# Performance work log

Hardware: AMD Instinct MI355X
Metric: run time of the kernel (lower is better)

The kernel has to match this reference:

```python
import jax, jax.numpy as jnp
import numpy as np

H = 12          # num attention heads
D_HEAD = 64     # head size (768 / 12)
P = 2           # power-law exponent
C = 5.0         # score shift
EPS = 1e-10


def setup_inputs() -> dict:
    key = jax.random.key(0)
    ks = jax.random.split(key, 8)
    B, S, Dm = 32, 512, 768
    scale = 1.0 / np.sqrt(Dm)
    return {
        "hidden_states": jax.random.normal(ks[0], (B, S, Dm), dtype=jnp.float32),
        "attention_mask": jnp.ones((B, 1, 1, S), dtype=jnp.float32),
        "Wq": jax.random.normal(ks[1], (Dm, Dm), dtype=jnp.float32) * scale,
        "bq": jnp.zeros((Dm,), dtype=jnp.float32),
        "Wk": jax.random.normal(ks[2], (Dm, Dm), dtype=jnp.float32) * scale,
        "bk": jnp.zeros((Dm,), dtype=jnp.float32),
        "Wv": jax.random.normal(ks[3], (Dm, Dm), dtype=jnp.float32) * scale,
        "bv": jnp.zeros((Dm,), dtype=jnp.float32),
    }


def _heads(x, B, S):
    # [B, S, H*d] -> [B, H, S, d]
    return x.reshape(B, S, H, D_HEAD).transpose(0, 2, 1, 3)


def reference(hidden_states, attention_mask, Wq, bq, Wk, bk, Wv, bv):
    B, S, Dm = hidden_states.shape
    q = _heads(hidden_states @ Wq + bq, B, S)
    k = _heads(hidden_states @ Wk + bk, B, S)
    v = _heads(hidden_states @ Wv + bv, B, S)

    inv_sqrt_d = 1.0 / (np.sqrt(D_HEAD) + 1e-10)
    scores = jnp.einsum("bhqd,bhkd->bhqk", q, k) * inv_sqrt_d  # [B,H,S,S]

    # Power-law attention (Powerformer, distill=0 branch)
    probs = jnp.power(scores + C, P)
    probs = probs / (jnp.sum(probs, axis=-1, keepdims=True) + EPS)
    probs = probs * attention_mask  # mask multiplied after normalization

    ctx = jnp.einsum("bhqk,bhkd->bhqd", probs, v)  # [B,H,S,d]
    ctx = ctx.transpose(0, 2, 1, 3).reshape(B, S, Dm)
    return ctx
```

## Files before the change

### kernel.cpp

```cpp
#include <hip/hip_runtime.h>

typedef __attribute__((ext_vector_type(8))) _Float16 half8;
typedef __attribute__((ext_vector_type(4))) _Float16 half4;
typedef __attribute__((ext_vector_type(4))) float f32x4;

#define MFMA_K32(a, b, c) __builtin_amdgcn_mfma_f32_16x16x32_f16((a), (b), (c), 0, 0, 0)
#define MFMA_K16(a, b, c) __builtin_amdgcn_mfma_f32_16x16x16f16((a), (b), (c), 0, 0, 0)

__device__ inline void async16(const _Float16* g, _Float16* l) {
    __builtin_amdgcn_global_load_lds(
        (const __attribute__((address_space(1))) void*)g,
        (__attribute__((address_space(3))) void*)l, 16, 0, 0);
}


__global__ __launch_bounds__(256) void xcast(const float* __restrict__ X,
                                             _Float16* __restrict__ Xh)
{
    size_t idx = ((size_t)blockIdx.x * 256 + threadIdx.x) * 8;
    float4 a = *(const float4*)(X + idx);
    float4 c = *(const float4*)(X + idx + 4);
    half8 hv;
    hv[0] = (_Float16)a.x; hv[1] = (_Float16)a.y;
    hv[2] = (_Float16)a.z; hv[3] = (_Float16)a.w;
    hv[4] = (_Float16)c.x; hv[5] = (_Float16)c.y;
    hv[6] = (_Float16)c.z; hv[7] = (_Float16)c.w;
    *(half8*)(Xh + idx) = hv;
}

__global__ __launch_bounds__(256) void wcast_kernel(
    const float* __restrict__ W0, const float* __restrict__ W1,
    const float* __restrict__ W2,
    _Float16* __restrict__ T0, _Float16* __restrict__ T1,
    _Float16* __restrict__ T2)
{
    int z = blockIdx.z;
    const float* W = (z == 0) ? W0 : (z == 1) ? W1 : W2;
    _Float16* T = (z == 0) ? T0 : (z == 1) ? T1 : T2;
    __shared__ float tile[32][33];
    int n0 = blockIdx.x * 32, k0 = blockIdx.y * 32;
    int tx = threadIdx.x & 31, ty = threadIdx.x >> 5;
#pragma unroll
    for (int r = 0; r < 4; ++r)
        tile[ty + 8 * r][tx] = W[(size_t)(k0 + ty + 8 * r) * 768 + n0 + tx];
    __syncthreads();
#pragma unroll
    for (int r = 0; r < 4; ++r)
        T[(size_t)(n0 + ty + 8 * r) * 768 + k0 + tx] =
            (_Float16)tile[tx][ty + 8 * r];
}

__global__ __launch_bounds__(256) void qkv_gemm(
    const _Float16* __restrict__ Xh,
    const _Float16* __restrict__ W0, const _Float16* __restrict__ W1,
    const _Float16* __restrict__ W2,
    const float* __restrict__ b0, const float* __restrict__ b1,
    const float* __restrict__ b2,
    const float* __restrict__ mask,
    _Float16* __restrict__ Qo, _Float16* __restrict__ Ko,
    _Float16* __restrict__ Vo)
{
    int z = blockIdx.y / 6;
    int n0 = (blockIdx.y % 6) * 128;
    int m0 = blockIdx.x * 128;
    const _Float16* Wt = (z == 0) ? W0 : (z == 1) ? W1 : W2;
    const float* bias = (z == 0) ? b0 : (z == 1) ? b1 : b2;

    __shared__ __attribute__((aligned(16))) _Float16 As[128 * 64];
    __shared__ __attribute__((aligned(16))) _Float16 Bs[128 * 64];

    int t = threadIdx.x;
    int wave = t >> 6, lane = t & 63, quad = lane >> 4, l16 = lane & 15;
    int wm = (wave & 1) * 64, wn = (wave >> 1) * 64;

    int srow = t >> 3;
    int sg = (t & 7) ^ (srow & 7);

    const _Float16* gA = Xh + (size_t)(m0 + srow) * 768 + sg * 8;
    const _Float16* gB = Wt + (size_t)(n0 + srow) * 768 + sg * 8;
    _Float16* lA = As + t * 8;
    _Float16* lB = Bs + t * 8;

    f32x4 acc[4][4] = {};

    for (int k0 = 0; k0 < 768; k0 += 64) {
#pragma unroll
        for (int q = 0; q < 4; ++q) {
            async16(gA + (size_t)q * 32 * 768 + k0, lA + q * 2048);
            async16(gB + (size_t)q * 32 * 768 + k0, lB + q * 2048);
        }
        __syncthreads();
#pragma unroll
        for (int ks = 0; ks < 2; ++ks) {
            half8 af[4], bf[4];
#pragma unroll
            for (int i = 0; i < 4; ++i) {
                int row = wm + i * 16 + l16;
                af[i] = *(const half8*)&As[row * 64 +
                                           (((ks << 2) + quad) ^ (row & 7)) * 8];
            }
#pragma unroll
            for (int j = 0; j < 4; ++j) {
                int row = wn + j * 16 + l16;
                bf[j] = *(const half8*)&Bs[row * 64 +
                                           (((ks << 2) + quad) ^ (row & 7)) * 8];
            }
#pragma unroll
            for (int i = 0; i < 4; ++i)
#pragma unroll
                for (int j = 0; j < 4; ++j)
                    acc[i][j] = MFMA_K32(af[i], bf[j], acc[i][j]);
        }
        __syncthreads();
    }

    float mk[4][4];
    if (z == 2) {
#pragma unroll
        for (int i = 0; i < 4; ++i) {
            int mbase = m0 + wm + i * 16 + quad * 4;
            int bb = mbase >> 9, s = mbase & 511;
#pragma unroll
            for (int r = 0; r < 4; ++r)
                mk[i][r] = mask[(size_t)bb * 512 + s + r];
        }
    }
#pragma unroll
    for (int j = 0; j < 4; ++j) {
        int n = n0 + wn + j * 16 + l16;
        float bv = bias[n];
        int hh = n >> 6, d = n & 63;
#pragma unroll
        for (int i = 0; i < 4; ++i) {
            int mbase = m0 + wm + i * 16 + quad * 4;
            int bb = mbase >> 9, s = mbase & 511;
            if (z == 0) {
#pragma unroll
                for (int r = 0; r < 4; ++r) {
                    size_t off = (((size_t)(bb * 12 + hh)) * 512 + s + r) * 64 + d;
                    Qo[off] = (_Float16)((acc[i][j][r] + bv) * 0.125f);
                }
            } else if (z == 1) {
#pragma unroll
                for (int r = 0; r < 4; ++r) {
                    size_t off = (((size_t)(bb * 12 + hh)) * 512 + s + r) * 64 + d;
                    Ko[off] = (_Float16)(acc[i][j][r] + bv);
                }
            } else {
                half4 pk;
#pragma unroll
                for (int r = 0; r < 4; ++r)
                    pk[r] = (_Float16)((acc[i][j][r] + bv) * mk[i][r]);
                size_t off = (((size_t)(bb * 12 + hh)) * 64 + d) * 512 + s;
                *(half4*)&Vo[off] = pk;
            }
        }
    }
}

__global__ __launch_bounds__(256) void attn_kernel(
    const _Float16* __restrict__ Q, const _Float16* __restrict__ K,
    const _Float16* __restrict__ Vt, float* __restrict__ out)
{
    __shared__ __attribute__((aligned(16))) _Float16 Ks[2][64 * 88];
    __shared__ __attribute__((aligned(16))) _Float16 Vs[2][64 * 88];

    int t = threadIdx.x;
    int wave = t >> 6, lane = t & 63, quad = lane >> 4, l16 = lane & 15;
    int h = blockIdx.y, b = blockIdx.z;
    size_t bh = (size_t)b * 12 + h;
    const _Float16* Qp = Q + bh * (512 * 64);
    const _Float16* Kp = K + bh * (512 * 64);
    const _Float16* Vp = Vt + bh * (64 * 512);
    int qbase = blockIdx.x * 256 + wave * 64;

    half8 qf[4][2];
#pragma unroll
    for (int i = 0; i < 4; ++i)
#pragma unroll
        for (int ks = 0; ks < 2; ++ks)
            qf[i][ks] = *(const half8*)(Qp + (size_t)(qbase + i * 16 + l16) * 64 +
                                        ks * 32 + quad * 8);

    f32x4 ctx[4][4] = {};
    f32x4 rsum[4] = {};
    const half4 ones = {(_Float16)1.f, (_Float16)1.f, (_Float16)1.f, (_Float16)1.f};

    int srow = t >> 2, spart = (t & 3) * 16;
    const _Float16* kgb = Kp + (size_t)srow * 64 + spart;
    const _Float16* vgb = Vp + (size_t)srow * 512 + spart;

    half8 ka0 = *(const half8*)(kgb);
    half8 ka1 = *(const half8*)(kgb + 8);
    half8 va0 = *(const half8*)(vgb);
    half8 va1 = *(const half8*)(vgb + 8);
    *(half8*)&Ks[0][srow * 88 + spart] = ka0;
    *(half8*)&Ks[0][srow * 88 + spart + 8] = ka1;
    *(half8*)&Vs[0][srow * 88 + spart] = va0;
    *(half8*)&Vs[0][srow * 88 + spart + 8] = va1;
    __syncthreads();

    for (int kt = 0; kt < 8; ++kt) {
        int c = kt & 1;
        if (kt < 7) {
            size_t ko = (size_t)(kt + 1) * 64;
            ka0 = *(const half8*)(kgb + ko * 64);
            ka1 = *(const half8*)(kgb + ko * 64 + 8);
            va0 = *(const half8*)(vgb + ko);
            va1 = *(const half8*)(vgb + ko + 8);
        }

        __builtin_amdgcn_s_setprio(1);
#pragma unroll
        for (int kb = 0; kb < 4; ++kb) {
            half8 kf0 = *(const half8*)&Ks[c][(kb * 16 + l16) * 88 + quad * 8];
            half8 kf1 = *(const half8*)&Ks[c][(kb * 16 + l16) * 88 + 32 + quad * 8];
            f32x4 sc[4];
#pragma unroll
            for (int i = 0; i < 4; ++i) {
                f32x4 s0 = {0.f, 0.f, 0.f, 0.f};
                s0 = MFMA_K32(kf0, qf[i][0], s0);
                sc[i] = MFMA_K32(kf1, qf[i][1], s0);
            }
            half4 pA[4];
#pragma unroll
            for (int i = 0; i < 4; ++i) {
#pragma unroll
                for (int r = 0; r < 4; ++r) {
                    float s = sc[i][r] + 5.0f;
                    pA[i][r] = (_Float16)(s * s);
                }
            }
#pragma unroll
            for (int i = 0; i < 4; ++i)
                rsum[i] = MFMA_K16(pA[i], ones, rsum[i]);
#pragma unroll
            for (int n = 0; n < 4; ++n) {
                half4 vf = *(const half4*)&Vs[c][(n * 16 + l16) * 88 + kb * 16 + quad * 4];
#pragma unroll
                for (int i = 0; i < 4; ++i)
                    ctx[i][n] = MFMA_K16(pA[i], vf, ctx[i][n]);
            }
        }
        __builtin_amdgcn_s_setprio(0);

        if (kt < 7) {
            *(half8*)&Ks[1 - c][srow * 88 + spart] = ka0;
            *(half8*)&Ks[1 - c][srow * 88 + spart + 8] = ka1;
            *(half8*)&Vs[1 - c][srow * 88 + spart] = va0;
            *(half8*)&Vs[1 - c][srow * 88 + spart + 8] = va1;
        }
        __syncthreads();
    }

#pragma unroll
    for (int i = 0; i < 4; ++i) {
        f32x4 inv;
#pragma unroll
        for (int r = 0; r < 4; ++r)
            inv[r] = 1.0f / (rsum[i][r] + 1e-10f);
#pragma unroll
        for (int n = 0; n < 4; ++n)
#pragma unroll
            for (int r = 0; r < 4; ++r) {
                int q = qbase + i * 16 + quad * 4 + r;
                int d = n * 16 + l16;
                out[((size_t)b * 512 + q) * 768 + h * 64 + d] =
                    ctx[i][n][r] * inv[r];
            }
    }
}

extern "C" void kernel_launch(void* const* d_in, const int* in_sizes, int n_in,
                              void* d_out, int out_size, void* d_ws, size_t ws_size,
                              hipStream_t stream)
{
    const float* hs   = (const float*)d_in[0];
    const float* mask = (const float*)d_in[1];
    const float* Wq   = (const float*)d_in[2];
    const float* bq   = (const float*)d_in[3];
    const float* Wk   = (const float*)d_in[4];
    const float* bk   = (const float*)d_in[5];
    const float* Wv   = (const float*)d_in[6];
    const float* bv   = (const float*)d_in[7];
    float* out = (float*)d_out;

    char* ws = (char*)d_ws;
    _Float16* Wtq = (_Float16*)ws;
    _Float16* Wtk = Wtq + 768 * 768;
    _Float16* Wtv = Wtk + 768 * 768;
    _Float16* Qb  = Wtv + 768 * 768;
    _Float16* Kb  = Qb + 16384 * 768;
    _Float16* Vb  = Kb + 16384 * 768;
    _Float16* Xh = (_Float16*)d_out;

    xcast<<<dim3(6144), 256, 0, stream>>>(hs, Xh);
    wcast_kernel<<<dim3(24, 24, 3), 256, 0, stream>>>(Wq, Wk, Wv, Wtq, Wtk, Wtv);
    qkv_gemm<<<dim3(128, 18), 256, 0, stream>>>(Xh, Wtq, Wtk, Wtv,
                                                bq, bk, bv, mask, Qb, Kb, Vb);
    attn_kernel<<<dim3(2, 12, 32), 256, 0, stream>>>(Qb, Kb, Vb, out);
}
```

Measured before the change: 240.2 us.

## Stream K/V tiles via async global-to-LDS loads with XOR-swizzled layout

Replaces the register-staged K/V tile copies, which loaded into registers and then stored to padded LDS, with direct global_load_lds async transfers into unpadded 64-wide tiles. An XOR swizzle on 16-byte chunks replaces the padding to avoid LDS bank conflicts, and the MFMA fragment reads are reindexed to match. This frees registers and removes the explicit LDS store phase. It relies on the async loads being complete by the barrier at the end of each iteration, since there is no explicit vmcnt wait.

```diff
diff --git a/kernel.cpp b/kernel.cpp
--- a/kernel.cpp
+++ b/kernel.cpp
@@ -162,8 +162,8 @@
     const _Float16* __restrict__ Q, const _Float16* __restrict__ K,
     const _Float16* __restrict__ Vt, float* __restrict__ out)
 {
-    __shared__ __attribute__((aligned(16))) _Float16 Ks[2][64 * 88];
-    __shared__ __attribute__((aligned(16))) _Float16 Vs[2][64 * 88];
+    __shared__ __attribute__((aligned(16))) _Float16 Ks[2][64 * 64];
+    __shared__ __attribute__((aligned(16))) _Float16 Vs[2][64 * 64];
 
     int t = threadIdx.x;
     int wave = t >> 6, lane = t & 63, quad = lane >> 4, l16 = lane & 15;
@@ -186,35 +186,41 @@
     f32x4 rsum[4] = {};
     const half4 ones = {(_Float16)1.f, (_Float16)1.f, (_Float16)1.f, (_Float16)1.f};
 
-    int srow = t >> 2, spart = (t & 3) * 16;
-    const _Float16* kgb = Kp + (size_t)srow * 64 + spart;
-    const _Float16* vgb = Vp + (size_t)srow * 512 + spart;
-
-    half8 ka0 = *(const half8*)(kgb);
-    half8 ka1 = *(const half8*)(kgb + 8);
-    half8 va0 = *(const half8*)(vgb);
-    half8 va1 = *(const half8*)(vgb + 8);
-    *(half8*)&Ks[0][srow * 88 + spart] = ka0;
-    *(half8*)&Ks[0][srow * 88 + spart + 8] = ka1;
-    *(half8*)&Vs[0][srow * 88 + spart] = va0;
-    *(half8*)&Vs[0][srow * 88 + spart + 8] = va1;
+    int srow0 = t >> 3;
+    int sg = (t & 7) ^ (srow0 & 7);
+    const _Float16* kg = Kp + (size_t)srow0 * 64 + sg * 8;
+    const _Float16* vg = Vp + (size_t)srow0 * 512 + sg * 8;
+    _Float16* lK = (_Float16*)Ks + t * 8;
+    _Float16* lV = (_Float16*)Vs + t * 8;
+
+    async16(kg, lK);
+    async16(kg + 2048, lK + 2048);
+    async16(vg, lV);
+    async16(vg + 16384, lV + 2048);
     __syncthreads();
+
+    int pswz = quad ^ (l16 & 7);
+    int vc   = (quad >> 1) ^ (l16 & 7);
+    int vsub = (quad & 1) * 4;
 
     for (int kt = 0; kt < 8; ++kt) {
         int c = kt & 1;
         if (kt < 7) {
-            size_t ko = (size_t)(kt + 1) * 64;
-            ka0 = *(const half8*)(kgb + ko * 64);
-            ka1 = *(const half8*)(kgb + ko * 64 + 8);
-            va0 = *(const half8*)(vgb + ko);
-            va1 = *(const half8*)(vgb + ko + 8);
-        }
-
+            int nb = 1 - c;
+            async16(kg + (kt + 1) * 4096, lK + nb * 4096);
+            async16(kg + (kt + 1) * 4096 + 2048, lK + nb * 4096 + 2048);
+            async16(vg + (kt + 1) * 64, lV + nb * 4096);
+            async16(vg + (kt + 1) * 64 + 16384, lV + nb * 4096 + 2048);
+        }
+
+        const _Float16* Kc = Ks[c];
+        const _Float16* Vc = Vs[c];
         __builtin_amdgcn_s_setprio(1);
 #pragma unroll
         for (int kb = 0; kb < 4; ++kb) {
-            half8 kf0 = *(const half8*)&Ks[c][(kb * 16 + l16) * 88 + quad * 8];
-            half8 kf1 = *(const half8*)&Ks[c][(kb * 16 + l16) * 88 + 32 + quad * 8];
+            int krow = kb * 16 + l16;
+            half8 kf0 = *(const half8*)&Kc[krow * 64 + pswz * 8];
+            half8 kf1 = *(const half8*)&Kc[krow * 64 + (pswz ^ 4) * 8];
             f32x4 sc[4];
 #pragma unroll
             for (int i = 0; i < 4; ++i) {
@@ -236,20 +242,15 @@
                 rsum[i] = MFMA_K16(pA[i], ones, rsum[i]);
 #pragma unroll
             for (int n = 0; n < 4; ++n) {
-                half4 vf = *(const half4*)&Vs[c][(n * 16 + l16) * 88 + kb * 16 + quad * 4];
+                half4 vf = *(const half4*)&Vc[(n * 16 + l16) * 64 +
+                                              ((2 * kb + (quad >> 1)) ^ (l16 & 7)) * 8 +
+                                              vsub];
 #pragma unroll
                 for (int i = 0; i < 4; ++i)
                     ctx[i][n] = MFMA_K16(pA[i], vf, ctx[i][n]);
             }
         }
         __builtin_amdgcn_s_setprio(0);
-
-        if (kt < 7) {
-            *(half8*)&Ks[1 - c][srow * 88 + spart] = ka0;
-            *(half8*)&Ks[1 - c][srow * 88 + spart + 8] = ka1;
-            *(half8*)&Vs[1 - c][srow * 88 + spart] = va0;
-            *(half8*)&Vs[1 - c][srow * 88 + spart + 8] = va1;
-        }
         __syncthreads();
     }
 
```

After: 245.6 us. 2.3% more time.
